# Kernel tuning notes

Hardware: AMD Instinct MI355X
Metric: run time of the kernel (lower is better)

## Reference

```python
import jax, jax.numpy as jnp
import numpy as np

K = 3          # attention window (kernel_size)
PAD = 1        # padding
C_IN = 256
C_OUT = 512    # final_channel
N_SPECIES, N_FAMILY, N_ORDER = 64500, 510, 100


def setup_inputs() -> dict:
    key = jax.random.key(0)
    ks = jax.random.split(key, 16)
    B, H, W = 4, 64, 64
    std = 0.01  # per torch.nn.init.normal_(std=0.01)
    inp = {
        "x": jax.random.normal(ks[0], (B, C_IN, H, W), jnp.float32),
        "wq": jax.random.normal(ks[1], (C_OUT, C_IN), jnp.float32) * std,
        "bq": jnp.zeros((C_OUT,), jnp.float32),
        "wk": jax.random.normal(ks[2], (C_OUT, C_IN), jnp.float32) * std,
        "bk": jnp.zeros((C_OUT,), jnp.float32),
        "wv": jax.random.normal(ks[3], (C_OUT, C_IN), jnp.float32) * std,
        "bv": jnp.zeros((C_OUT,), jnp.float32),
        "rel_h": jax.random.normal(ks[4], (C_OUT // 2, K), jnp.float32),
        "rel_w": jax.random.normal(ks[5], (C_OUT // 2, K), jnp.float32),
        "w_species": jax.random.normal(ks[6], (N_SPECIES, C_OUT), jnp.float32) * std,
        "b_species": jnp.zeros((N_SPECIES,), jnp.float32),
        "w_family": jax.random.normal(ks[7], (N_FAMILY, C_OUT), jnp.float32) * std,
        "b_family": jnp.zeros((N_FAMILY,), jnp.float32),
        "w_order": jax.random.normal(ks[8], (N_ORDER, C_OUT), jnp.float32) * std,
        "b_order": jnp.zeros((N_ORDER,), jnp.float32),
    }
    return inp


def _patches(t, H, W):
    # t: padded [B, C, H+2, W+2] -> [B, C, H, W, K, K] (unfold order: kh then kw)
    return jnp.stack([
        jnp.stack([t[:, :, i:i + H, j:j + W] for j in range(K)], axis=-1)
        for i in range(K)], axis=-2)


def _attention_conv(x, wq, bq, wk, bk, wv, bv, rel_h, rel_w):
    B, _, H, W = x.shape
    q = jnp.einsum('oc,bchw->bohw', wq, x) + bq[None, :, None, None]
    k = jnp.einsum('oc,bchw->bohw', wk, x) + bk[None, :, None, None]
    v = jnp.einsum('oc,bchw->bohw', wv, x) + bv[None, :, None, None]
    pad = ((0, 0), (0, 0), (PAD, PAD), (PAD, PAD))
    kp = _patches(jnp.pad(k, pad), H, W)                       # [B,C,H,W,K,K]
    vp = _patches(jnp.pad(v, pad), H, W).reshape(B, C_OUT, H, W, K * K)
    half = C_OUT // 2
    kp = jnp.concatenate([
        kp[:, :half] + rel_h[None, :, None, None, :, None],    # rel over kh
        kp[:, half:] + rel_w[None, :, None, None, None, :],    # rel over kw
    ], axis=1).reshape(B, C_OUT, H, W, K * K)
    attn = jax.nn.softmax(q[..., None] * kp, axis=-1)          # per-channel softmax over window
    return jnp.einsum('bchwk,bchwk->bchw', attn, vp)


def reference(x, wq, bq, wk, bk, wv, bv, rel_h, rel_w,
              w_species, b_species, w_family, b_family, w_order, b_order):
    att = jax.nn.relu(_attention_conv(x, wq, bq, wk, bk, wv, bv, rel_h, rel_w))
    pooled = att.mean(axis=(2, 3))                             # AdaptiveAvgPool2d((1,1)) -> [B, 512]
    sp = pooled @ w_species.T + b_species
    fa = pooled @ w_family.T + b_family
    od = pooled @ w_order.T + b_order
    # concatenated per-level logits (species | family | order)
    return jnp.concatenate([sp, fa, od], axis=1)
```

## Files before the change

### kernel.cpp

```cpp
#include <hip/hip_runtime.h>
#include <stdint.h>

#define HW    4096
#define CIN   256
#define COUT  512
#define NSPE  64500
#define NFAM  510
#define NORD  100
#define NOUT  65110

typedef __attribute__((ext_vector_type(8))) short bf16x8;
typedef __attribute__((ext_vector_type(4))) float f32x4;
typedef __attribute__((address_space(3))) uint32_t lds_u32;
typedef __attribute__((address_space(1))) const uint32_t glob_u32;

__device__ __forceinline__ short f32_to_bf16(float f) {
    uint32_t u = __float_as_uint(f);
    u += 0x7fffu + ((u >> 16) & 1u);
    return (short)(u >> 16);
}
__device__ __forceinline__ float bf16_to_f32(unsigned short s) {
    return __uint_as_float(((uint32_t)s) << 16);
}


__global__ __launch_bounds__(256) void convert_w_kernel(
    const float* __restrict__ wq, const float* __restrict__ wk,
    const float* __restrict__ wv, short* __restrict__ Wt)
{
    const int kt = blockIdx.x, mt = blockIdx.y, mat = blockIdx.z;
    const float* __restrict__ W = (mat == 0) ? wq : (mat == 1) ? wk : wv;
    const int t = threadIdx.x;
    const int m = t >> 1;
    short* out = Wt + (((size_t)(mat * 4 + mt) * 8 + kt) << 12);

    union { short s[16]; int4 v[2]; } pk;
    #pragma unroll
    for (int j = 0; j < 16; ++j) {
        int e  = t * 16 + j;
        int sp = (e >> 3) & 3;
        int i  = e & 7;
        int k  = ((sp ^ ((m >> 1) & 3)) << 3) + i;
        pk.s[j] = f32_to_bf16(W[(size_t)(mt * 128 + m) * CIN + kt * 32 + k]);
    }
    int4* dst = (int4*)(out + t * 16);
    dst[0] = pk.v[0];
    dst[1] = pk.v[1];
}

__global__ __launch_bounds__(256) void convert_x_kernel(
    const float* __restrict__ x, short* __restrict__ Xt)
{
    const int kt = blockIdx.x, nt = blockIdx.y, b = blockIdx.z;
    const int t = threadIdx.x;
    __shared__ float lds[32][128];

    #pragma unroll
    for (int j = 0; j < 16; ++j) {
        int idx = j * 256 + t;
        int c = idx >> 7, p = idx & 127;
        lds[c][p] = x[((size_t)b * CIN + kt * 32 + c) * HW + nt * 128 + p];
    }
    __syncthreads();

    const int n = t >> 1;
    short* out = Xt + (((size_t)(b * 32 + nt) * 8 + kt) << 12);
    union { short s[16]; int4 v[2]; } pk;
    #pragma unroll
    for (int j = 0; j < 16; ++j) {
        int e  = t * 16 + j;
        int sp = (e >> 3) & 3;
        int i  = e & 7;
        int k  = ((sp ^ ((n >> 1) & 3)) << 3) + i;
        pk.s[j] = f32_to_bf16(lds[k][n]);
    }
    int4* dst = (int4*)(out + t * 16);
    dst[0] = pk.v[0];
    dst[1] = pk.v[1];
}

__global__ __launch_bounds__(256) void qkv_mfma_kernel(
    const short* __restrict__ Wt, const short* __restrict__ Xt,
    const float* __restrict__ bq, const float* __restrict__ bk,
    const float* __restrict__ bv, short* __restrict__ qkv)
{
    const int nt = blockIdx.x, mt = blockIdx.y, z = blockIdx.z;
    const int mat = z >> 2, b = z & 3;
    const short* At = Wt + (((size_t)(mat * 4 + mt) * 8) << 12);
    const short* Bt = Xt + (((size_t)(b * 32 + nt) * 8) << 12);

    __shared__ __align__(16) short As[4096];
    __shared__ __align__(16) short Bs[4096];

    const int tid = threadIdx.x, lane = tid & 63, wid = tid >> 6;
    const int wm = wid >> 1, wn = wid & 1;
    const int l15 = lane & 15, sl = lane >> 4;
    const int sw = ((sl ^ ((l15 >> 1) & 3)) << 3);

    f32x4 acc[4][4] = {};

    for (int kt = 0; kt < 8; ++kt) {
        #pragma unroll
        for (int j = 0; j < 4; ++j) {
            int li = wid * 4 + j;
            if (li < 8)
                __builtin_amdgcn_global_load_lds(
                    (glob_u32*)(At + kt * 4096 + li * 512 + lane * 8),
                    (lds_u32*)(As + li * 512), 16, 0, 0);
            else
                __builtin_amdgcn_global_load_lds(
                    (glob_u32*)(Bt + kt * 4096 + (li - 8) * 512 + lane * 8),
                    (lds_u32*)(Bs + (li - 8) * 512), 16, 0, 0);
        }
        __syncthreads();

        bf16x8 a[4], bb[4];
        #pragma unroll
        for (int f = 0; f < 4; ++f) {
            int ra = wm * 64 + f * 16 + l15;
            a[f]  = *(const bf16x8*)(As + ra * 32 + sw);
            int rb = wn * 64 + f * 16 + l15;
            bb[f] = *(const bf16x8*)(Bs + rb * 32 + sw);
        }
        #pragma unroll
        for (int mf = 0; mf < 4; ++mf)
            #pragma unroll
            for (int nf = 0; nf < 4; ++nf)
                acc[mf][nf] = __builtin_amdgcn_mfma_f32_16x16x32_bf16(
                    a[mf], bb[nf], acc[mf][nf], 0, 0, 0);
        __syncthreads();
    }

    const float* bias = (mat == 0) ? bq : (mat == 1) ? bk : bv;
    short* out = qkv + (((size_t)(b * 3 + mat) * COUT + mt * 128) * HW) + nt * 128;
    const int col = lane & 15, g = lane >> 4;
    #pragma unroll
    for (int mf = 0; mf < 4; ++mf) {
        #pragma unroll
        for (int nf = 0; nf < 4; ++nf) {
            #pragma unroll
            for (int r = 0; r < 4; ++r) {
                int m = wm * 64 + mf * 16 + g * 4 + r;
                int n = wn * 64 + nf * 16 + col;
                float val = acc[mf][nf][r] + bias[mt * 128 + m];
                out[(size_t)m * HW + n] = f32_to_bf16(val);
            }
        }
    }
}

__global__ __launch_bounds__(256) void attn_pool_kernel(
    const unsigned short* __restrict__ qkv,
    const float* __restrict__ rel_h, const float* __restrict__ rel_w,
    float* __restrict__ pooled)
{
    const int c = blockIdx.x;
    const int b = blockIdx.y;
    const int tid = threadIdx.x;
    const int h  = tid >> 2;
    const int w0 = (tid & 3) * 16;

    const unsigned short* qc = qkv + ((size_t)(b * 3 + 0) * COUT + c) * HW;
    const unsigned short* kc = qkv + ((size_t)(b * 3 + 1) * COUT + c) * HW;
    const unsigned short* vc = qkv + ((size_t)(b * 3 + 2) * COUT + c) * HW;

    __shared__ __align__(16) unsigned short kS[64 * 72];
    __shared__ __align__(16) unsigned short vS[64 * 72];

    #pragma unroll
    for (int it = 0; it < 2; ++it) {
        int ch = tid + it * 256;
        int y = ch >> 3, off = (ch & 7) * 8;
        *(int4*)&kS[y * 72 + off] = reinterpret_cast<const int4*>(kc)[ch];
        *(int4*)&vS[y * 72 + off] = reinterpret_cast<const int4*>(vc)[ch];
    }

    union { unsigned short s[16]; int4 v[2]; } qr;
    qr.v[0] = reinterpret_cast<const int4*>(qc + h * 64 + w0)[0];
    qr.v[1] = reinterpret_cast<const int4*>(qc + h * 64 + w0)[1];
    float qf[16];
    #pragma unroll
    for (int i = 0; i < 16; ++i) qf[i] = bf16_to_f32(qr.s[i]);

    const bool isH = (c < 256);
    float r3[3];
    #pragma unroll
    for (int i = 0; i < 3; ++i)
        r3[i] = isH ? rel_h[c * 3 + i] : rel_w[(c - 256) * 3 + i];

    __syncthreads();

    float total = 0.f;
    #pragma unroll
    for (int i = 0; i < 16; ++i) {
        const int w = w0 + i;
        const float qv = qf[i];
        float s[9], vv9[9];
        #pragma unroll
        for (int kh = 0; kh < 3; ++kh) {
            const int y = h + kh - 1;
            const bool rowok = ((unsigned)y < 64u);
            const int yc = rowok ? y : h;
            #pragma unroll
            for (int kw = 0; kw < 3; ++kw) {
                const int xw = w + kw - 1;
                const bool ok = rowok && ((unsigned)xw < 64u);
                const int xc = ((unsigned)xw < 64u) ? xw : w;
                float kval = bf16_to_f32(kS[yc * 72 + xc]);
                float vval = bf16_to_f32(vS[yc * 72 + xc]);
                kval = ok ? kval : 0.f;
                vval = ok ? vval : 0.f;
                const float rel = isH ? r3[kh] : r3[kw];
                s[kh * 3 + kw]   = qv * (kval + rel);
                vv9[kh * 3 + kw] = vval;
            }
        }
        float m = s[0];
        #pragma unroll
        for (int t = 1; t < 9; ++t) m = fmaxf(m, s[t]);
        float den = 0.f, num = 0.f;
        #pragma unroll
        for (int t = 0; t < 9; ++t) {
            float e = __expf(s[t] - m);
            den += e;
            num += e * vv9[t];
        }
        total += fmaxf(num / den, 0.f);
    }

    #pragma unroll
    for (int off = 32; off; off >>= 1) total += __shfl_down(total, off);
    __shared__ float red[4];
    if ((tid & 63) == 0) red[tid >> 6] = total;
    __syncthreads();
    if (tid == 0)
        pooled[b * COUT + c] = (red[0] + red[1] + red[2] + red[3]) * (1.f / 4096.f);
}

__global__ __launch_bounds__(256) void heads_kernel(
    const float* __restrict__ pooled,
    const float* __restrict__ w_sp, const float* __restrict__ b_sp,
    const float* __restrict__ w_fa, const float* __restrict__ b_fa,
    const float* __restrict__ w_or, const float* __restrict__ b_or,
    float* __restrict__ out)
{
    const int lane   = threadIdx.x & 63;
    const int wave   = blockIdx.x * (blockDim.x >> 6) + (threadIdx.x >> 6);
    const int nwaves = gridDim.x * (blockDim.x >> 6);

    float pr[4][8];
    #pragma unroll
    for (int b = 0; b < 4; ++b)
        #pragma unroll
        for (int e = 0; e < 8; ++e)
            pr[b][e] = pooled[b * COUT + lane * 8 + e];

    for (int j = wave; j < NOUT; j += nwaves) {
        const float* __restrict__ wrow;
        float bias;
        if (j < NSPE)            { wrow = w_sp + (size_t)j * COUT;          bias = b_sp[j]; }
        else if (j < NSPE + NFAM){ wrow = w_fa + (size_t)(j - NSPE) * COUT; bias = b_fa[j - NSPE]; }
        else                     { wrow = w_or + (size_t)(j - NSPE - NFAM) * COUT; bias = b_or[j - NSPE - NFAM]; }

        const float4 w0 = reinterpret_cast<const float4*>(wrow)[lane * 2 + 0];
        const float4 w1 = reinterpret_cast<const float4*>(wrow)[lane * 2 + 1];
        const float we[8] = {w0.x, w0.y, w0.z, w0.w, w1.x, w1.y, w1.z, w1.w};

        float a0 = 0.f, a1 = 0.f, a2 = 0.f, a3 = 0.f;
        #pragma unroll
        for (int e = 0; e < 8; ++e) {
            a0 += we[e] * pr[0][e];
            a1 += we[e] * pr[1][e];
            a2 += we[e] * pr[2][e];
            a3 += we[e] * pr[3][e];
        }
        #pragma unroll
        for (int off = 32; off; off >>= 1) {
            a0 += __shfl_down(a0, off);
            a1 += __shfl_down(a1, off);
            a2 += __shfl_down(a2, off);
            a3 += __shfl_down(a3, off);
        }
        if (lane == 0) {
            out[0 * NOUT + j] = a0 + bias;
            out[1 * NOUT + j] = a1 + bias;
            out[2 * NOUT + j] = a2 + bias;
            out[3 * NOUT + j] = a3 + bias;
        }
    }
}

extern "C" void kernel_launch(void* const* d_in, const int* in_sizes, int n_in,
                              void* d_out, int out_size, void* d_ws, size_t ws_size,
                              hipStream_t stream) {
    const float* x     = (const float*)d_in[0];
    const float* wq    = (const float*)d_in[1];
    const float* bq    = (const float*)d_in[2];
    const float* wk    = (const float*)d_in[3];
    const float* bk    = (const float*)d_in[4];
    const float* wv    = (const float*)d_in[5];
    const float* bv    = (const float*)d_in[6];
    const float* rel_h = (const float*)d_in[7];
    const float* rel_w = (const float*)d_in[8];
    const float* w_sp  = (const float*)d_in[9];
    const float* b_sp  = (const float*)d_in[10];
    const float* w_fa  = (const float*)d_in[11];
    const float* b_fa  = (const float*)d_in[12];
    const float* w_or  = (const float*)d_in[13];
    const float* b_or  = (const float*)d_in[14];
    float* out = (float*)d_out;

    short* Wt  = (short*)d_ws;
    short* Xt  = Wt + 393216;
    short* qkv = Xt + 4194304;
    float* pooled = (float*)(qkv + 25165824);

    convert_w_kernel<<<dim3(8, 4, 3), 256, 0, stream>>>(wq, wk, wv, Wt);
    convert_x_kernel<<<dim3(8, 32, 4), 256, 0, stream>>>(x, Xt);
    qkv_mfma_kernel<<<dim3(32, 4, 12), 256, 0, stream>>>(Wt, Xt, bq, bk, bv, qkv);
    attn_pool_kernel<<<dim3(COUT, 4), 256, 0, stream>>>(
        (const unsigned short*)qkv, rel_h, rel_w, pooled);
    heads_kernel<<<dim3(1024), 256, 0, stream>>>(
        pooled, w_sp, b_sp, w_fa, b_fa, w_or, b_or, out);
}
```

Measured before the change: 86.39 us.

## Double-buffer QKV GEMM loads and streamline attention window softmax

The QKV MFMA kernel now double-buffers its LDS tiles, issuing the next k-tile's global-to-LDS loads before computing on the current one. The attention kernel stores K/V as fp32 in a zero-padded LDS tile, so the per-element boundary checks disappear. It also reuses a sliding 3-column window of registers, drops the max-subtraction, and uses exp2 with q pre-scaled by log2(e) plus a fast reciprocal. The heads kernel grid is doubled. Skipping the max-subtraction risks overflow if the scores grow large, and the single barrier per iteration in the double buffer relies on load ordering.

```diff
diff --git a/kernel.cpp b/kernel.cpp
--- a/kernel.cpp
+++ b/kernel.cpp
@@ -89,8 +89,8 @@
     const short* At = Wt + (((size_t)(mat * 4 + mt) * 8) << 12);
     const short* Bt = Xt + (((size_t)(b * 32 + nt) * 8) << 12);
 
-    __shared__ __align__(16) short As[4096];
-    __shared__ __align__(16) short Bs[4096];
+    __shared__ __align__(16) short As[2][4096];
+    __shared__ __align__(16) short Bs[2][4096];
 
     const int tid = threadIdx.x, lane = tid & 63, wid = tid >> 6;
     const int wm = wid >> 1, wn = wid & 1;
@@ -99,28 +99,36 @@
 
     f32x4 acc[4][4] = {};
 
+#define STAGE(KT, BUF) do {                                                   \
+    _Pragma("unroll")                                                         \
+    for (int j = 0; j < 4; ++j) {                                             \
+        int li = wid * 4 + j;                                                 \
+        if (li < 8)                                                           \
+            __builtin_amdgcn_global_load_lds(                                 \
+                (glob_u32*)(At + (KT) * 4096 + li * 512 + lane * 8),          \
+                (lds_u32*)(&As[BUF][li * 512]), 16, 0, 0);                    \
+        else                                                                  \
+            __builtin_amdgcn_global_load_lds(                                 \
+                (glob_u32*)(Bt + (KT) * 4096 + (li - 8) * 512 + lane * 8),    \
+                (lds_u32*)(&Bs[BUF][(li - 8) * 512]), 16, 0, 0);              \
+    }                                                                         \
+} while (0)
+
+    STAGE(0, 0);
+    __syncthreads();
+
+    int buf = 0;
+    #pragma unroll 2
     for (int kt = 0; kt < 8; ++kt) {
-        #pragma unroll
-        for (int j = 0; j < 4; ++j) {
-            int li = wid * 4 + j;
-            if (li < 8)
-                __builtin_amdgcn_global_load_lds(
-                    (glob_u32*)(At + kt * 4096 + li * 512 + lane * 8),
-                    (lds_u32*)(As + li * 512), 16, 0, 0);
-            else
-                __builtin_amdgcn_global_load_lds(
-                    (glob_u32*)(Bt + kt * 4096 + (li - 8) * 512 + lane * 8),
-                    (lds_u32*)(Bs + (li - 8) * 512), 16, 0, 0);
-        }
-        __syncthreads();
+        if (kt < 7) STAGE(kt + 1, buf ^ 1);
 
         bf16x8 a[4], bb[4];
         #pragma unroll
         for (int f = 0; f < 4; ++f) {
             int ra = wm * 64 + f * 16 + l15;
-            a[f]  = *(const bf16x8*)(As + ra * 32 + sw);
+            a[f]  = *(const bf16x8*)(&As[buf][ra * 32 + sw]);
             int rb = wn * 64 + f * 16 + l15;
-            bb[f] = *(const bf16x8*)(Bs + rb * 32 + sw);
+            bb[f] = *(const bf16x8*)(&Bs[buf][rb * 32 + sw]);
         }
         #pragma unroll
         for (int mf = 0; mf < 4; ++mf)
@@ -129,7 +137,9 @@
                 acc[mf][nf] = __builtin_amdgcn_mfma_f32_16x16x32_bf16(
                     a[mf], bb[nf], acc[mf][nf], 0, 0, 0);
         __syncthreads();
-    }
+        buf ^= 1;
+    }
+#undef STAGE
 
     const float* bias = (mat == 0) ? bq : (mat == 1) ? bk : bv;
     short* out = qkv + (((size_t)(b * 3 + mat) * COUT + mt * 128) * HW) + nt * 128;
@@ -161,18 +171,36 @@
     const int w0 = (tid & 3) * 16;
 
     const unsigned short* qc = qkv + ((size_t)(b * 3 + 0) * COUT + c) * HW;
-    const unsigned short* kc = qkv + ((size_t)(b * 3 + 1) * COUT + c) * HW;
-    const unsigned short* vc = qkv + ((size_t)(b * 3 + 2) * COUT + c) * HW;
-
-    __shared__ __align__(16) unsigned short kS[64 * 72];
-    __shared__ __align__(16) unsigned short vS[64 * 72];
+    const unsigned short* kg = qkv + ((size_t)(b * 3 + 1) * COUT + c) * HW;
+    const unsigned short* vg = qkv + ((size_t)(b * 3 + 2) * COUT + c) * HW;
+
+    __shared__ float kS[66 * 67];
+    __shared__ float vS[66 * 67];
+
+    if (tid < 67) {
+        kS[tid] = 0.f;            vS[tid] = 0.f;
+        kS[65 * 67 + tid] = 0.f;  vS[65 * 67 + tid] = 0.f;
+    }
+    if (tid < 64) {
+        int r0 = (tid + 1) * 67;
+        kS[r0] = 0.f;       vS[r0] = 0.f;
+        kS[r0 + 65] = 0.f;  vS[r0 + 65] = 0.f;
+    }
 
     #pragma unroll
     for (int it = 0; it < 2; ++it) {
         int ch = tid + it * 256;
-        int y = ch >> 3, off = (ch & 7) * 8;
-        *(int4*)&kS[y * 72 + off] = reinterpret_cast<const int4*>(kc)[ch];
-        *(int4*)&vS[y * 72 + off] = reinterpret_cast<const int4*>(vc)[ch];
+        int y = ch >> 3, xs = (ch & 7) * 8;
+        union { int4 v; unsigned short s[8]; } ak, av;
+        ak.v = reinterpret_cast<const int4*>(kg)[ch];
+        av.v = reinterpret_cast<const int4*>(vg)[ch];
+        float* kp = &kS[(y + 1) * 67 + xs + 1];
+        float* vp = &vS[(y + 1) * 67 + xs + 1];
+        #pragma unroll
+        for (int e = 0; e < 8; ++e) {
+            kp[e] = bf16_to_f32(ak.s[e]);
+            vp[e] = bf16_to_f32(av.s[e]);
+        }
     }
 
     union { unsigned short s[16]; int4 v[2]; } qr;
@@ -180,52 +208,56 @@
     qr.v[1] = reinterpret_cast<const int4*>(qc + h * 64 + w0)[1];
     float qf[16];
     #pragma unroll
-    for (int i = 0; i < 16; ++i) qf[i] = bf16_to_f32(qr.s[i]);
+    for (int i = 0; i < 16; ++i)
+        qf[i] = bf16_to_f32(qr.s[i]) * 1.4426950408889634f;
 
     const bool isH = (c < 256);
     float r3[3];
     #pragma unroll
     for (int i = 0; i < 3; ++i)
         r3[i] = isH ? rel_h[c * 3 + i] : rel_w[(c - 256) * 3 + i];
+    float relv[9];
+    #pragma unroll
+    for (int kh = 0; kh < 3; ++kh)
+        #pragma unroll
+        for (int kw = 0; kw < 3; ++kw)
+            relv[kh * 3 + kw] = isH ? r3[kh] : r3[kw];
 
     __syncthreads();
 
+    const float* krow = &kS[h * 67 + w0];
+    const float* vrow = &vS[h * 67 + w0];
+
+    float kcw[3][3], vcw[3][3];
+    #pragma unroll
+    for (int s = 0; s < 2; ++s)
+        #pragma unroll
+        for (int r = 0; r < 3; ++r) {
+            kcw[s][r] = krow[r * 67 + s];
+            vcw[s][r] = vrow[r * 67 + s];
+        }
+
     float total = 0.f;
     #pragma unroll
     for (int i = 0; i < 16; ++i) {
-        const int w = w0 + i;
-        const float qv = qf[i];
-        float s[9], vv9[9];
-        #pragma unroll
-        for (int kh = 0; kh < 3; ++kh) {
-            const int y = h + kh - 1;
-            const bool rowok = ((unsigned)y < 64u);
-            const int yc = rowok ? y : h;
+        const int s2 = (i + 2) % 3;
+        #pragma unroll
+        for (int r = 0; r < 3; ++r) {
+            kcw[s2][r] = krow[r * 67 + i + 2];
+            vcw[s2][r] = vrow[r * 67 + i + 2];
+        }
+        const float q2 = qf[i];
+        float num = 0.f, den = 0.f;
+        #pragma unroll
+        for (int r = 0; r < 3; ++r)
             #pragma unroll
-            for (int kw = 0; kw < 3; ++kw) {
-                const int xw = w + kw - 1;
-                const bool ok = rowok && ((unsigned)xw < 64u);
-                const int xc = ((unsigned)xw < 64u) ? xw : w;
-                float kval = bf16_to_f32(kS[yc * 72 + xc]);
-                float vval = bf16_to_f32(vS[yc * 72 + xc]);
-                kval = ok ? kval : 0.f;
-                vval = ok ? vval : 0.f;
-                const float rel = isH ? r3[kh] : r3[kw];
-                s[kh * 3 + kw]   = qv * (kval + rel);
-                vv9[kh * 3 + kw] = vval;
+            for (int dx = 0; dx < 3; ++dx) {
+                const int sl = (i + dx) % 3;
+                float e = __builtin_exp2f(q2 * (kcw[sl][r] + relv[r * 3 + dx]));
+                den += e;
+                num = fmaf(e, vcw[sl][r], num);
             }
-        }
-        float m = s[0];
-        #pragma unroll
-        for (int t = 1; t < 9; ++t) m = fmaxf(m, s[t]);
-        float den = 0.f, num = 0.f;
-        #pragma unroll
-        for (int t = 0; t < 9; ++t) {
-            float e = __expf(s[t] - m);
-            den += e;
-            num += e * vv9[t];
-        }
-        total += fmaxf(num / den, 0.f);
+        total += fmaxf(num * __builtin_amdgcn_rcpf(den), 0.f);
     }
 
     #pragma unroll
@@ -320,6 +352,6 @@
     qkv_mfma_kernel<<<dim3(32, 4, 12), 256, 0, stream>>>(Wt, Xt, bq, bk, bv, qkv);
     attn_pool_kernel<<<dim3(COUT, 4), 256, 0, stream>>>(
         (const unsigned short*)qkv, rel_h, rel_w, pooled);
-    heads_kernel<<<dim3(1024), 256, 0, stream>>>(
+    heads_kernel<<<dim3(2048), 256, 0, stream>>>(
         pooled, w_sp, b_sp, w_fa, b_fa, w_or, b_or, out);
 }
```

New measurement: 84.96 us. No clear change (-1.7%).
